# Kernel optimization log

Hardware: AMD Instinct MI355X
Metric: run time of the kernel (lower is better)

Reference implementation:

```python
import jax, jax.numpy as jnp
import numpy as np

E, H, I, T, K = 8, 2048, 1024, 4096, 2
GROUP = 32


def dequant_int4(packed, scale, group):
    """packed: [E, R, C//2] ints in [0,256) holding two 4-bit values per byte.
    scale: [E, R, C//group]. Returns fp32 [E, R, C] with w = (nibble - 8) * scale."""
    lo = (packed & 0xF) - 8          # even columns
    hi = ((packed >> 4) & 0xF) - 8   # odd columns
    e, r, ch = packed.shape
    w = jnp.stack([lo, hi], axis=-1).reshape(e, r, 2 * ch).astype(jnp.float32)
    w = w.reshape(e, r, -1, group) * scale[..., None]
    return w.reshape(e, r, 2 * ch)


def setup_inputs() -> dict:
    key = jax.random.key(0)
    ks = jax.random.split(key, 6)
    x = jax.random.normal(ks[0], (T, H), dtype=jnp.float32)
    w1 = jax.random.randint(ks[1], (E, 2 * I, H // 2), 0, 256, dtype=jnp.int32)
    w1_scale = jax.random.uniform(ks[2], (E, 2 * I, H // GROUP), dtype=jnp.float32) * 0.02
    w2 = jax.random.randint(ks[3], (E, H, I // 2), 0, 256, dtype=jnp.int32)
    w2_scale = jax.random.uniform(ks[4], (E, H, I // GROUP), dtype=jnp.float32) * 0.02
    logits = jax.random.normal(ks[5], (T, E), dtype=jnp.float32)
    top_vals, top_idx = jax.lax.top_k(logits, K)
    expert_weights = jax.nn.softmax(top_vals, axis=-1)   # [T, K]
    expert_indices = top_idx.astype(jnp.int32)           # [T, K]
    return {"x": x, "w1": w1, "w1_scale": w1_scale, "w2": w2,
            "w2_scale": w2_scale, "expert_weights": expert_weights,
            "expert_indices": expert_indices, "top_k": K}


def reference(x, w1, w1_scale, w2, w2_scale, expert_weights, expert_indices, top_k):
    inter = w2.shape[2] * 2
    W1 = dequant_int4(w1, w1_scale, GROUP)   # [E, 2I, H]
    W2 = dequant_int4(w2, w2_scale, GROUP)   # [E, H, I]
    y13 = jnp.einsum('th,erh->etr', x, W1)   # [E, T, 2I]
    gate, up = y13[..., :inter], y13[..., inter:]
    h = jax.nn.silu(gate) * up               # [E, T, I] SwiGLU
    y = jnp.einsum('eti,ehi->eth', h, W2)    # [E, T, H]
    t_ids = jnp.arange(x.shape[0])[:, None]  # [T, 1]
    sel = y[expert_indices, t_ids, :]        # [T, K, H]
    return jnp.einsum('tkh,tk->th', sel, expert_weights)
```

## Files before the change

kernel.cpp:

```cpp
#include <hip/hip_runtime.h>
#include <cstdint>
#include <cstddef>

typedef unsigned int u32;
typedef unsigned short u16;
typedef __bf16 bf16x8 __attribute__((ext_vector_type(8)));
typedef float f32x4 __attribute__((ext_vector_type(4)));
typedef u16 u16x8 __attribute__((ext_vector_type(8)));

static constexpr int T_TOK = 4096;
static constexpr int HID   = 2048;
static constexpr int INTER = 1024;
static constexpr int NEXP  = 8;
static constexpr int TOPK  = 2;
static constexpr int SLOT_CAP = 10240;
static constexpr int NT_M = 40;

static constexpr int M_TOT  = 16;
static constexpr int M_CUR  = 17;
static constexpr int M_DONE = 40;
static constexpr int M_TOK  = 96;

__device__ __forceinline__ u16 f2bf(float f) {
  u32 u = __builtin_bit_cast(u32, f);
  u32 r = (u + 0x7fffu + ((u >> 16) & 1u)) >> 16;
  return (u16)r;
}
__device__ __forceinline__ float bf2f(u16 h) {
  return __builtin_bit_cast(float, (u32)h << 16);
}

__device__ __forceinline__ void spin_ge(int* p, int target) {
  while (__hip_atomic_load(p, __ATOMIC_RELAXED, __HIP_MEMORY_SCOPE_AGENT) < target)
    __builtin_amdgcn_s_sleep(8);
  __builtin_amdgcn_fence(__ATOMIC_ACQUIRE, "agent");
}
__device__ __forceinline__ void bump(int* p, int tid) {
  __syncthreads();
  if (tid == 0)
    __hip_atomic_fetch_add(p, 1, __ATOMIC_RELEASE, __HIP_MEMORY_SCOPE_AGENT);
}

__global__ void router_count(const int* __restrict__ eidx, int* __restrict__ meta) {
  __shared__ int cnt[NEXP];
  const int tid = threadIdx.x;
  if (tid < NEXP) cnt[tid] = 0;
  __syncthreads();
  for (int i = tid; i < T_TOK * TOPK; i += 256) atomicAdd(&cnt[eidx[i]], 1);
  __syncthreads();
  if (tid == 0) {
    int off = 0;
    for (int e = 0; e < NEXP; ++e) {
      int c = cnt[e];
      meta[e] = c;
      meta[8 + e] = off;
      meta[M_CUR + e] = off;
      off += (c + 255) & ~255;
    }
    meta[M_TOT] = off;
  }
}

__global__ void init_k(int* __restrict__ meta) {
  const int i = blockIdx.x * 256 + threadIdx.x;
  if (i < SLOT_CAP) meta[M_TOK + i] = 0;
  if (i >= 25 && i < 80) meta[i] = 0;
}

__global__ void router_assign(const int* __restrict__ eidx, int* __restrict__ meta) {
  const int t = blockIdx.x * 256 + threadIdx.x;
  if (t >= T_TOK) return;
  int* cursors = meta + M_CUR;
  int* toklist = meta + M_TOK;
  for (int k = 0; k < TOPK; ++k) {
    const int e = eidx[t * TOPK + k];
    const int pos = atomicAdd(&cursors[e], 1);
    toklist[pos] = t * 2 + k;
  }
}

template <int CPR>
__device__ __forceinline__ void deq1(const int* __restrict__ p, const float* __restrict__ s,
                                     u16* __restrict__ w, int gid) {
  const int row = gid / CPR;
  const int cid = gid % CPR;
  const int4 pk = *(const int4*)(p + (size_t)gid * 4);
  const float sc = s[(size_t)row * (CPR / 4) + (cid >> 2)];
  int v[4] = {pk.x, pk.y, pk.z, pk.w};
  u16x8 o;
#pragma unroll
  for (int b = 0; b < 4; ++b) {
    o[2 * b]     = f2bf((float)((v[b] & 15) - 8) * sc);
    o[2 * b + 1] = f2bf((float)(((v[b] >> 4) & 15) - 8) * sc);
  }
  *(u16x8*)(w + (size_t)gid * 8) = o;
}

__global__ void prep_k(const int* __restrict__ w1, const float* __restrict__ w1s,
                       const int* __restrict__ w2, const float* __restrict__ w2s,
                       const float* __restrict__ x, u16* __restrict__ W1b,
                       u16* __restrict__ W2b, u16* __restrict__ xb) {
  const int blk = blockIdx.x;
  if (blk < 16384) {
    deq1<256>(w1, w1s, W1b, blk * 256 + threadIdx.x);
  } else if (blk < 24576) {
    deq1<128>(w2, w2s, W2b, (blk - 16384) * 256 + threadIdx.x);
  } else {
    const int i = ((blk - 24576) * 256 + threadIdx.x) * 8;
    const float4 a = *(const float4*)(x + i);
    const float4 b = *(const float4*)(x + i + 4);
    u16x8 o;
    o[0] = f2bf(a.x); o[1] = f2bf(a.y); o[2] = f2bf(a.z); o[3] = f2bf(a.w);
    o[4] = f2bf(b.x); o[5] = f2bf(b.y); o[6] = f2bf(b.z); o[7] = f2bf(b.w);
    *(u16x8*)(xb + i) = o;
  }
}

template <int KT, bool G1M>
__device__ void gemm_body(const u16* __restrict__ A, const u16* __restrict__ Be,
                          u16* __restrict__ Cout, const int* __restrict__ toklist,
                          int vend, u16* lds, int slot0, int nt, int tid) {
  static constexpr int NT = KT / 64;
  char* ldsB = (char*)lds;

  const u16* asrc[4];
  const u16* bsrc[4];
#pragma unroll
  for (int j = 0; j < 4; ++j) {
    const int L = j * 8192 + tid * 16;
    const int S = L >> 10;
    int o = L & 1023;
    o ^= ((o >> 7) & 3) << 4;
    const int r = (S >> 1) * 16 + (o >> 6);
    const int cb = (S & 1) * 64 + (o & 63);
    const int arow = G1M ? (toklist[slot0 + r] >> 1) : (slot0 + r);
    asrc[j] = A + (size_t)arow * KT + (cb >> 1);
    int brow;
    if (G1M) {
      const int g = r >> 6, j6 = r & 63;
      brow = nt * 128 + g * 32 + (j6 & 31) + ((j6 >> 5) << 10);
    } else {
      brow = nt * 256 + r;
    }
    bsrc[j] = Be + (size_t)brow * KT + (cb >> 1);
  }

#define STAGE(kt_, c_)                                                                \
  do {                                                                                \
    char* dA_ = ldsB + (c_) * 65536;                                                  \
    char* dB_ = dA_ + 32768;                                                          \
    _Pragma("unroll") for (int j = 0; j < 4; ++j)                                     \
        __builtin_amdgcn_global_load_lds(                                             \
            (const __attribute__((address_space(1))) void*)(asrc[j] + (kt_) * 64),    \
            (__attribute__((address_space(3))) void*)(dA_ + j * 8192 + tid * 16),     \
            16, 0, 0);                                                                \
    _Pragma("unroll") for (int j = 0; j < 4; ++j)                                     \
        __builtin_amdgcn_global_load_lds(                                             \
            (const __attribute__((address_space(1))) void*)(bsrc[j] + (kt_) * 64),    \
            (__attribute__((address_space(3))) void*)(dB_ + j * 8192 + tid * 16),     \
            16, 0, 0);                                                                \
  } while (0)

  const int lane = tid & 63;
  const int wid = tid >> 6;
  const int wm = (wid >> 2) * 128;
  const int wn = (wid & 3) * 64;
  const int fr = lane & 15;
  const int qq = lane >> 4;
  const int swz = (qq * 16) ^ (((fr >> 1) & 3) << 4);

  const int abase = (wm >> 4) * 2048 + fr * 64 + swz;
  const int bbase = 32768 + (wn >> 4) * 2048 + fr * 64 + swz;

  f32x4 acc[8][4];
#pragma unroll
  for (int m = 0; m < 8; ++m)
#pragma unroll
    for (int n = 0; n < 4; ++n) acc[m][n] = (f32x4)0.0f;

#define COMPUTE(c_)                                                                   \
  do {                                                                                \
    const char* bb_ = ldsB + (c_) * 65536;                                            \
    bf16x8 bfr_[4][2];                                                                \
    _Pragma("unroll") for (int nf = 0; nf < 4; ++nf)                                  \
        _Pragma("unroll") for (int ks = 0; ks < 2; ++ks)                              \
            bfr_[nf][ks] = *(const bf16x8*)(bb_ + bbase + nf * 2048 + ks * 1024);     \
    _Pragma("unroll") for (int mh = 0; mh < 2; ++mh) {                                \
      bf16x8 af_[4][2];                                                               \
      _Pragma("unroll") for (int mf = 0; mf < 4; ++mf)                                \
          _Pragma("unroll") for (int ks = 0; ks < 2; ++ks)                            \
              af_[mf][ks] = *(const bf16x8*)(bb_ + abase + mh * 8192 + mf * 2048 +    \
                                             ks * 1024);                              \
      __builtin_amdgcn_s_setprio(1);                                                  \
      _Pragma("unroll") for (int mf = 0; mf < 4; ++mf)                                \
          _Pragma("unroll") for (int nf = 0; nf < 4; ++nf)                            \
              _Pragma("unroll") for (int ks = 0; ks < 2; ++ks)                        \
                  acc[mh * 4 + mf][nf] = __builtin_amdgcn_mfma_f32_16x16x32_bf16(     \
                      af_[mf][ks], bfr_[nf][ks], acc[mh * 4 + mf][nf], 0, 0, 0);      \
      __builtin_amdgcn_s_setprio(0);                                                  \
    }                                                                                 \
  } while (0)

  STAGE(0, 0);
#pragma unroll 1
  for (int kt = 0; kt < NT; kt += 2) {
    asm volatile("s_waitcnt vmcnt(0)" ::: "memory");
    __builtin_amdgcn_s_barrier();
    __builtin_amdgcn_sched_barrier(0);
    if (kt + 1 < NT) STAGE(kt + 1, 1);
    COMPUTE(0);
    asm volatile("s_waitcnt vmcnt(0)" ::: "memory");
    __builtin_amdgcn_s_barrier();
    __builtin_amdgcn_sched_barrier(0);
    if (kt + 2 < NT) STAGE(kt + 2, 0);
    COMPUTE(1);
  }
#undef STAGE
#undef COMPUTE

  if (G1M) {
    const int g = wid & 3;
#pragma unroll
    for (int mi = 0; mi < 8; ++mi)
#pragma unroll
      for (int n = 0; n < 2; ++n)
#pragma unroll
        for (int jj = 0; jj < 4; ++jj) {
          const float gv = acc[mi][n][jj];
          const float uv = acc[mi][n + 2][jj];
          const float hv = gv / (1.0f + __expf(-gv)) * uv;
          const int row = slot0 + wm + mi * 16 + qq * 4 + jj;
          Cout[(size_t)row * INTER + nt * 128 + g * 32 + n * 16 + fr] = f2bf(hv);
        }
  } else {
#pragma unroll
    for (int mi = 0; mi < 8; ++mi)
#pragma unroll
      for (int jj = 0; jj < 4; ++jj) {
        const int slot = slot0 + wm + mi * 16 + qq * 4 + jj;
        if (slot < vend) {
          const int tk = toklist[slot];
          const int col = nt * 256 + wn + fr;
#pragma unroll
          for (int n = 0; n < 4; ++n)
            Cout[(size_t)tk * HID + col + n * 16] = f2bf(acc[mi][n][jj]);
        }
      }
  }
}

__device__ __forceinline__ void run_g1(const u16* xb, const u16* W1b, u16* hbuf,
                                       int* meta, const int* toklist, u16* lds,
                                       int mt, int nt, int tid) {
  const int slot0 = mt * 256;
  if (slot0 < meta[M_TOT]) {
    int e = 0;
#pragma unroll
    for (int i = 1; i < NEXP; ++i) e += (slot0 >= meta[8 + i]);
    gemm_body<2048, true>(xb, W1b + (size_t)e * 2048 * 2048, hbuf, toklist, 0,
                          lds, slot0, nt, tid);
  }
  bump(&meta[M_DONE + mt], tid);
}

__device__ __forceinline__ void run_g2(const u16* hbuf, const u16* W2b, u16* yt,
                                       int* meta, const int* toklist, u16* lds,
                                       int mt, int nt, int tid) {
  const int slot0 = mt * 256;
  if (slot0 >= meta[M_TOT]) return;
  int e = 0;
#pragma unroll
  for (int i = 1; i < NEXP; ++i) e += (slot0 >= meta[8 + i]);
  if (tid == 0) spin_ge(&meta[M_DONE + mt], 8);
  __syncthreads();
  const int vend = meta[8 + e] + meta[e];
  gemm_body<1024, false>(hbuf, W2b + (size_t)e * 2048 * 1024, yt, toklist, vend,
                         lds, slot0, nt, tid);
}

__global__ __launch_bounds__(512, 2) void gemm_static(
    const u16* __restrict__ xb, const u16* __restrict__ W1b,
    const u16* __restrict__ W2b, u16* __restrict__ hbuf, u16* __restrict__ yt,
    int* __restrict__ meta) {
  __shared__ u16 lds[2 * 32768];
  const int tid = threadIdx.x;
  const int b = blockIdx.x;
  const int* toklist = meta + M_TOK;

  run_g1(xb, W1b, hbuf, meta, toklist, lds, b & 31, b >> 5, tid);
  if (b < 64) {
    run_g1(xb, W1b, hbuf, meta, toklist, lds, 32 + (b & 7), b >> 3, tid);
    run_g2(hbuf, W2b, yt, meta, toklist, lds, 32 + (b & 7), b >> 3, tid);
  } else {
    const int x = b & 7, q = (b - 64) >> 3;
    {
      const int k = q;
      run_g2(hbuf, W2b, yt, meta, toklist, lds, x + 8 * (k & 3), k >> 2, tid);
    }
    if (q < 8) {
      const int k = q + 24;
      run_g2(hbuf, W2b, yt, meta, toklist, lds, x + 8 * (k & 3), k >> 2, tid);
    }
  }
}

__global__ void combine_k(const u16* __restrict__ yt, const float* __restrict__ ew,
                          float* __restrict__ out) {
  const int idx = blockIdx.x * 256 + threadIdx.x;
  const int t = idx >> 8;
  const int pos = (idx & 255) * 8;
  const float w0 = ew[t * 2];
  const float w1 = ew[t * 2 + 1];
  const u16x8 v0 = *(const u16x8*)(yt + (size_t)(t * 2) * HID + pos);
  const u16x8 v1 = *(const u16x8*)(yt + (size_t)(t * 2 + 1) * HID + pos);
  float* dst = out + (size_t)t * HID + pos;
  float4 o0, o1;
  o0.x = w0 * bf2f(v0[0]) + w1 * bf2f(v1[0]);
  o0.y = w0 * bf2f(v0[1]) + w1 * bf2f(v1[1]);
  o0.z = w0 * bf2f(v0[2]) + w1 * bf2f(v1[2]);
  o0.w = w0 * bf2f(v0[3]) + w1 * bf2f(v1[3]);
  o1.x = w0 * bf2f(v0[4]) + w1 * bf2f(v1[4]);
  o1.y = w0 * bf2f(v0[5]) + w1 * bf2f(v1[5]);
  o1.z = w0 * bf2f(v0[6]) + w1 * bf2f(v1[6]);
  o1.w = w0 * bf2f(v0[7]) + w1 * bf2f(v1[7]);
  *(float4*)dst = o0;
  *(float4*)(dst + 4) = o1;
}

extern "C" void kernel_launch(void* const* d_in, const int* in_sizes, int n_in,
                              void* d_out, int out_size, void* d_ws, size_t ws_size,
                              hipStream_t stream) {
  const float* x    = (const float*)d_in[0];
  const int*   w1   = (const int*)d_in[1];
  const float* w1s  = (const float*)d_in[2];
  const int*   w2   = (const int*)d_in[3];
  const float* w2s  = (const float*)d_in[4];
  const float* ew   = (const float*)d_in[5];
  const int*   eidx = (const int*)d_in[6];
  float* out = (float*)d_out;

  char* ws = (char*)d_ws;
  const size_t OFF_W1B  = 0;
  const size_t OFF_W2B  = 67108864;
  const size_t OFF_XB   = 100663296;
  const size_t OFF_H    = 117440512;
  const size_t OFF_YT   = 138412032;
  const size_t OFF_META = 171966464;
  const size_t NEED     = 172043264;
  if (ws_size < NEED) return;

  u16* W1b  = (u16*)(ws + OFF_W1B);
  u16* W2b  = (u16*)(ws + OFF_W2B);
  u16* xb   = (u16*)(ws + OFF_XB);
  u16* hbuf = (u16*)(ws + OFF_H);
  u16* yt   = (u16*)(ws + OFF_YT);
  int* meta = (int*)(ws + OFF_META);

  router_count<<<1, 256, 0, stream>>>(eidx, meta);
  init_k<<<SLOT_CAP / 256, 256, 0, stream>>>(meta);
  router_assign<<<T_TOK / 256, 256, 0, stream>>>(eidx, meta);

  prep_k<<<28672, 256, 0, stream>>>(w1, w1s, w2, w2s, x, W1b, W2b, xb);

  gemm_static<<<256, 512, 0, stream>>>(xb, W1b, W2b, hbuf, yt, meta);

  combine_k<<<(T_TOK * HID) / (256 * 8), 256, 0, stream>>>(yt, ew, out);
}
```

Baseline: 251.8 us.

## Interleave global-to-LDS staging with MFMA sub-blocks in ping-pong schedule

Replaces the two-stage loop (stage next tile, then compute the whole tile) with a finer schedule. Each k-tile's compute is split into four MFMA quarter blocks, with barriers between them, and the global_load_lds issues for the next tiles are spread across those quarters. Two tiles are prefetched up front and partial vmcnt waits are used, so memory traffic overlaps more evenly with matrix work. The loop now always issues loads with wrapped indices (masked by NT-1), which assumes NT is a power of two and adds redundant trailing loads. It also adds many more barriers.

```diff
diff --git a/kernel.cpp b/kernel.cpp
--- a/kernel.cpp
+++ b/kernel.cpp
@@ -145,21 +145,18 @@
     bsrc[j] = Be + (size_t)brow * KT + (cb >> 1);
   }
 
-#define STAGE(kt_, c_)                                                                \
-  do {                                                                                \
-    char* dA_ = ldsB + (c_) * 65536;                                                  \
-    char* dB_ = dA_ + 32768;                                                          \
-    _Pragma("unroll") for (int j = 0; j < 4; ++j)                                     \
-        __builtin_amdgcn_global_load_lds(                                             \
-            (const __attribute__((address_space(1))) void*)(asrc[j] + (kt_) * 64),    \
-            (__attribute__((address_space(3))) void*)(dA_ + j * 8192 + tid * 16),     \
-            16, 0, 0);                                                                \
-    _Pragma("unroll") for (int j = 0; j < 4; ++j)                                     \
-        __builtin_amdgcn_global_load_lds(                                             \
-            (const __attribute__((address_space(1))) void*)(bsrc[j] + (kt_) * 64),    \
-            (__attribute__((address_space(3))) void*)(dB_ + j * 8192 + tid * 16),     \
-            16, 0, 0);                                                                \
-  } while (0)
+#define STG_A(kt_, c_, j_)                                                          \
+  __builtin_amdgcn_global_load_lds(                                                 \
+      (const __attribute__((address_space(1))) void*)(asrc[j_] + (kt_) * 64),       \
+      (__attribute__((address_space(3))) void*)(ldsB + (c_) * 65536 + (j_) * 8192 + \
+                                                tid * 16),                           \
+      16, 0, 0)
+#define STG_B(kt_, c_, j_)                                                          \
+  __builtin_amdgcn_global_load_lds(                                                 \
+      (const __attribute__((address_space(1))) void*)(bsrc[j_] + (kt_) * 64),       \
+      (__attribute__((address_space(3))) void*)(ldsB + (c_) * 65536 + 32768 +       \
+                                                (j_) * 8192 + tid * 16),             \
+      16, 0, 0)
 
   const int lane = tid & 63;
   const int wid = tid >> 6;
@@ -178,45 +175,76 @@
 #pragma unroll
     for (int n = 0; n < 4; ++n) acc[m][n] = (f32x4)0.0f;
 
-#define COMPUTE(c_)                                                                   \
-  do {                                                                                \
-    const char* bb_ = ldsB + (c_) * 65536;                                            \
-    bf16x8 bfr_[4][2];                                                                \
-    _Pragma("unroll") for (int nf = 0; nf < 4; ++nf)                                  \
-        _Pragma("unroll") for (int ks = 0; ks < 2; ++ks)                              \
-            bfr_[nf][ks] = *(const bf16x8*)(bb_ + bbase + nf * 2048 + ks * 1024);     \
-    _Pragma("unroll") for (int mh = 0; mh < 2; ++mh) {                                \
-      bf16x8 af_[4][2];                                                               \
-      _Pragma("unroll") for (int mf = 0; mf < 4; ++mf)                                \
-          _Pragma("unroll") for (int ks = 0; ks < 2; ++ks)                            \
-              af_[mf][ks] = *(const bf16x8*)(bb_ + abase + mh * 8192 + mf * 2048 +    \
-                                             ks * 1024);                              \
-      __builtin_amdgcn_s_setprio(1);                                                  \
-      _Pragma("unroll") for (int mf = 0; mf < 4; ++mf)                                \
-          _Pragma("unroll") for (int nf = 0; nf < 4; ++nf)                            \
-              _Pragma("unroll") for (int ks = 0; ks < 2; ++ks)                        \
-                  acc[mh * 4 + mf][nf] = __builtin_amdgcn_mfma_f32_16x16x32_bf16(     \
-                      af_[mf][ks], bfr_[nf][ks], acc[mh * 4 + mf][nf], 0, 0, 0);      \
-      __builtin_amdgcn_s_setprio(0);                                                  \
-    }                                                                                 \
+  bf16x8 af[4][2], b01[2][2], b23[2][2];
+
+#define BARRIER asm volatile("s_barrier" ::: "memory")
+#define LGKM0                                              \
+  do {                                                     \
+    asm volatile("s_waitcnt lgkmcnt(0)" ::: "memory");     \
+    __builtin_amdgcn_sched_barrier(0);                     \
   } while (0)
-
-  STAGE(0, 0);
+#define DS_AF(c_, mh_)                                                              \
+  _Pragma("unroll") for (int mf = 0; mf < 4; ++mf)                                  \
+  _Pragma("unroll") for (int ks = 0; ks < 2; ++ks)                                  \
+      af[mf][ks] = *(const bf16x8*)(ldsB + (c_) * 65536 + abase + (mh_) * 8192 +    \
+                                    mf * 2048 + ks * 1024);
+#define DS_B(c_, bh_, BV_)                                                          \
+  _Pragma("unroll") for (int nf = 0; nf < 2; ++nf)                                  \
+  _Pragma("unroll") for (int ks = 0; ks < 2; ++ks)                                  \
+      BV_[nf][ks] = *(const bf16x8*)(ldsB + (c_) * 65536 + bbase +                  \
+                                     ((bh_) * 2 + nf) * 2048 + ks * 1024);
+#define MFMA16(mh_, bh_, BV_)                                                       \
+  do {                                                                              \
+    __builtin_amdgcn_s_setprio(1);                                                  \
+    _Pragma("unroll") for (int mf = 0; mf < 4; ++mf)                                \
+    _Pragma("unroll") for (int nf = 0; nf < 2; ++nf)                                \
+    _Pragma("unroll") for (int ks = 0; ks < 2; ++ks)                                \
+        acc[(mh_) * 4 + mf][(bh_) * 2 + nf] =                                       \
+            __builtin_amdgcn_mfma_f32_16x16x32_bf16(                                \
+                af[mf][ks], BV_[nf][ks], acc[(mh_) * 4 + mf][(bh_) * 2 + nf],       \
+                0, 0, 0);                                                           \
+    __builtin_amdgcn_s_setprio(0);                                                  \
+  } while (0)
+
+  STG_A(0, 0, 0); STG_A(0, 0, 2); STG_B(0, 0, 0); STG_B(0, 0, 1);
+  STG_B(0, 0, 2); STG_B(0, 0, 3); STG_A(0, 0, 1); STG_A(0, 0, 3);
+  STG_A(1, 1, 0); STG_A(1, 1, 2); STG_B(1, 1, 0); STG_B(1, 1, 1);
+  STG_B(1, 1, 2); STG_B(1, 1, 3); STG_A(1, 1, 1); STG_A(1, 1, 3);
+  asm volatile("s_waitcnt vmcnt(8)" ::: "memory");
+  BARRIER;
+
 #pragma unroll 1
-  for (int kt = 0; kt < NT; kt += 2) {
-    asm volatile("s_waitcnt vmcnt(0)" ::: "memory");
-    __builtin_amdgcn_s_barrier();
-    __builtin_amdgcn_sched_barrier(0);
-    if (kt + 1 < NT) STAGE(kt + 1, 1);
-    COMPUTE(0);
-    asm volatile("s_waitcnt vmcnt(0)" ::: "memory");
-    __builtin_amdgcn_s_barrier();
-    __builtin_amdgcn_sched_barrier(0);
-    if (kt + 2 < NT) STAGE(kt + 2, 0);
-    COMPUTE(1);
-  }
-#undef STAGE
-#undef COMPUTE
+  for (int it = 0; it < NT / 2; ++it) {
+    const int s0 = (2 * it + 2) & (NT - 1);
+    const int s1 = (2 * it + 3) & (NT - 1);
+    DS_AF(0, 0); DS_B(0, 0, b01);
+    BARRIER; LGKM0; MFMA16(0, 0, b01); BARRIER;
+    DS_B(0, 1, b23); STG_A(s0, 0, 0); STG_A(s0, 0, 2);
+    BARRIER; LGKM0; MFMA16(0, 1, b23); BARRIER;
+    DS_AF(0, 1); STG_B(s0, 0, 0); STG_B(s0, 0, 1);
+    BARRIER; LGKM0; MFMA16(1, 0, b01); BARRIER;
+    STG_B(s0, 0, 2); STG_B(s0, 0, 3);
+    BARRIER; MFMA16(1, 1, b23);
+    asm volatile("s_waitcnt vmcnt(6)" ::: "memory");
+    BARRIER;
+    DS_AF(1, 0); DS_B(1, 0, b01); STG_A(s0, 0, 1); STG_A(s0, 0, 3);
+    BARRIER; LGKM0; MFMA16(0, 0, b01); BARRIER;
+    DS_B(1, 1, b23); STG_A(s1, 1, 0); STG_A(s1, 1, 2);
+    BARRIER; LGKM0; MFMA16(0, 1, b23); BARRIER;
+    DS_AF(1, 1); STG_B(s1, 1, 0); STG_B(s1, 1, 1); STG_B(s1, 1, 2); STG_B(s1, 1, 3);
+    BARRIER; LGKM0; MFMA16(1, 0, b01); BARRIER;
+    STG_A(s1, 1, 1); STG_A(s1, 1, 3);
+    BARRIER; MFMA16(1, 1, b23);
+    asm volatile("s_waitcnt vmcnt(8)" ::: "memory");
+    BARRIER;
+  }
+#undef STG_A
+#undef STG_B
+#undef BARRIER
+#undef LGKM0
+#undef DS_AF
+#undef DS_B
+#undef MFMA16
 
   if (G1M) {
     const int g = wid & 3;
```

Result: no change. 256.1 us (+1.7%).

## Shrink fused MoE GEMM tiles to 128x128 with one-shot grid and per-tile sync

Applied to the files above, without the earlier changes.

Replaces the persistent 256-block, 256x256-tile schedule with a one-shot grid of 128x128 tiles on 256-thread blocks. Each block runs its gate/up GEMM tile, then waits on a per-row-tile counter before its down-projection tile. Expert slot padding drops from 256 to 128, which cuts wasted rows and exposes more parallel blocks. In exchange, the double-buffered LDS pipeline and MFMA priority hints are removed in favour of a single buffer with two barriers per k-step, so load latency is no longer hidden. Smaller tiles also give less operand reuse, and spinning blocks hold CU slots while they wait.

```diff
diff --git a/kernel.cpp b/kernel.cpp
--- a/kernel.cpp
+++ b/kernel.cpp
@@ -13,13 +13,14 @@
 static constexpr int INTER = 1024;
 static constexpr int NEXP  = 8;
 static constexpr int TOPK  = 2;
-static constexpr int SLOT_CAP = 10240;
-static constexpr int NT_M = 40;
+static constexpr int SLOT_CAP = 9216;
+static constexpr int NT_M = 72;
+static constexpr int NT_N = 16;
 
 static constexpr int M_TOT  = 16;
 static constexpr int M_CUR  = 17;
-static constexpr int M_DONE = 40;
-static constexpr int M_TOK  = 96;
+static constexpr int M_DONE = 128;
+static constexpr int M_TOK  = 256;
 
 __device__ __forceinline__ u16 f2bf(float f) {
   u32 u = __builtin_bit_cast(u32, f);
@@ -55,7 +56,7 @@
       meta[e] = c;
       meta[8 + e] = off;
       meta[M_CUR + e] = off;
-      off += (c + 255) & ~255;
+      off += (c + 127) & ~127;
     }
     meta[M_TOT] = off;
   }
@@ -64,7 +65,7 @@
 __global__ void init_k(int* __restrict__ meta) {
   const int i = blockIdx.x * 256 + threadIdx.x;
   if (i < SLOT_CAP) meta[M_TOK + i] = 0;
-  if (i >= 25 && i < 80) meta[i] = 0;
+  if (i >= M_DONE && i < M_DONE + NT_M) meta[i] = 0;
 }
 
 __global__ void router_assign(const int* __restrict__ eidx, int* __restrict__ meta) {
@@ -117,9 +118,9 @@
 }
 
 template <int KT, bool G1M>
-__device__ void gemm_body(const u16* __restrict__ A, const u16* __restrict__ Be,
-                          u16* __restrict__ Cout, const int* __restrict__ toklist,
-                          int vend, u16* lds, int slot0, int nt, int tid) {
+__device__ void tile128(const u16* __restrict__ A, const u16* __restrict__ Be,
+                        u16* __restrict__ Cout, const int* __restrict__ toklist,
+                        int vend, u16* lds, int slot0, int nt, int tid) {
   static constexpr int NT = KT / 64;
   char* ldsB = (char*)lds;
 
@@ -127,7 +128,7 @@
   const u16* bsrc[4];
 #pragma unroll
   for (int j = 0; j < 4; ++j) {
-    const int L = j * 8192 + tid * 16;
+    const int L = j * 4096 + tid * 16;
     const int S = L >> 10;
     int o = L & 1023;
     o ^= ((o >> 7) & 3) << 4;
@@ -137,171 +138,126 @@
     asrc[j] = A + (size_t)arow * KT + (cb >> 1);
     int brow;
     if (G1M) {
-      const int g = r >> 6, j6 = r & 63;
-      brow = nt * 128 + g * 32 + (j6 & 31) + ((j6 >> 5) << 10);
+      const int w = r >> 6, j6 = r & 63;
+      brow = (j6 < 32) ? (nt * 64 + w * 32 + j6)
+                       : (1024 + nt * 64 + w * 32 + (j6 & 31));
     } else {
-      brow = nt * 256 + r;
+      brow = nt * 128 + r;
     }
     bsrc[j] = Be + (size_t)brow * KT + (cb >> 1);
   }
 
-#define STAGE(kt_, c_)                                                                \
-  do {                                                                                \
-    char* dA_ = ldsB + (c_) * 65536;                                                  \
-    char* dB_ = dA_ + 32768;                                                          \
-    _Pragma("unroll") for (int j = 0; j < 4; ++j)                                     \
-        __builtin_amdgcn_global_load_lds(                                             \
-            (const __attribute__((address_space(1))) void*)(asrc[j] + (kt_) * 64),    \
-            (__attribute__((address_space(3))) void*)(dA_ + j * 8192 + tid * 16),     \
-            16, 0, 0);                                                                \
-    _Pragma("unroll") for (int j = 0; j < 4; ++j)                                     \
-        __builtin_amdgcn_global_load_lds(                                             \
-            (const __attribute__((address_space(1))) void*)(bsrc[j] + (kt_) * 64),    \
-            (__attribute__((address_space(3))) void*)(dB_ + j * 8192 + tid * 16),     \
-            16, 0, 0);                                                                \
-  } while (0)
-
   const int lane = tid & 63;
   const int wid = tid >> 6;
-  const int wm = (wid >> 2) * 128;
-  const int wn = (wid & 3) * 64;
+  const int wm = (wid >> 1) * 64;
+  const int wn = (wid & 1) * 64;
   const int fr = lane & 15;
   const int qq = lane >> 4;
   const int swz = (qq * 16) ^ (((fr >> 1) & 3) << 4);
 
   const int abase = (wm >> 4) * 2048 + fr * 64 + swz;
-  const int bbase = 32768 + (wn >> 4) * 2048 + fr * 64 + swz;
-
-  f32x4 acc[8][4];
-#pragma unroll
-  for (int m = 0; m < 8; ++m)
+  const int bbase = 16384 + (wn >> 4) * 2048 + fr * 64 + swz;
+
+  f32x4 acc[4][4];
+#pragma unroll
+  for (int m = 0; m < 4; ++m)
 #pragma unroll
     for (int n = 0; n < 4; ++n) acc[m][n] = (f32x4)0.0f;
 
-#define COMPUTE(c_)                                                                   \
-  do {                                                                                \
-    const char* bb_ = ldsB + (c_) * 65536;                                            \
-    bf16x8 bfr_[4][2];                                                                \
-    _Pragma("unroll") for (int nf = 0; nf < 4; ++nf)                                  \
-        _Pragma("unroll") for (int ks = 0; ks < 2; ++ks)                              \
-            bfr_[nf][ks] = *(const bf16x8*)(bb_ + bbase + nf * 2048 + ks * 1024);     \
-    _Pragma("unroll") for (int mh = 0; mh < 2; ++mh) {                                \
-      bf16x8 af_[4][2];                                                               \
-      _Pragma("unroll") for (int mf = 0; mf < 4; ++mf)                                \
-          _Pragma("unroll") for (int ks = 0; ks < 2; ++ks)                            \
-              af_[mf][ks] = *(const bf16x8*)(bb_ + abase + mh * 8192 + mf * 2048 +    \
-                                             ks * 1024);                              \
-      __builtin_amdgcn_s_setprio(1);                                                  \
-      _Pragma("unroll") for (int mf = 0; mf < 4; ++mf)                                \
-          _Pragma("unroll") for (int nf = 0; nf < 4; ++nf)                            \
-              _Pragma("unroll") for (int ks = 0; ks < 2; ++ks)                        \
-                  acc[mh * 4 + mf][nf] = __builtin_amdgcn_mfma_f32_16x16x32_bf16(     \
-                      af_[mf][ks], bfr_[nf][ks], acc[mh * 4 + mf][nf], 0, 0, 0);      \
-      __builtin_amdgcn_s_setprio(0);                                                  \
-    }                                                                                 \
-  } while (0)
-
-  STAGE(0, 0);
 #pragma unroll 1
-  for (int kt = 0; kt < NT; kt += 2) {
-    asm volatile("s_waitcnt vmcnt(0)" ::: "memory");
-    __builtin_amdgcn_s_barrier();
-    __builtin_amdgcn_sched_barrier(0);
-    if (kt + 1 < NT) STAGE(kt + 1, 1);
-    COMPUTE(0);
-    asm volatile("s_waitcnt vmcnt(0)" ::: "memory");
-    __builtin_amdgcn_s_barrier();
-    __builtin_amdgcn_sched_barrier(0);
-    if (kt + 2 < NT) STAGE(kt + 2, 0);
-    COMPUTE(1);
-  }
-#undef STAGE
-#undef COMPUTE
+  for (int kt = 0; kt < NT; ++kt) {
+    __syncthreads();
+#pragma unroll
+    for (int j = 0; j < 4; ++j) {
+      __builtin_amdgcn_global_load_lds(
+          (const __attribute__((address_space(1))) void*)(asrc[j] + kt * 64),
+          (__attribute__((address_space(3))) void*)(ldsB + j * 4096 + tid * 16),
+          16, 0, 0);
+      __builtin_amdgcn_global_load_lds(
+          (const __attribute__((address_space(1))) void*)(bsrc[j] + kt * 64),
+          (__attribute__((address_space(3))) void*)(ldsB + 16384 + j * 4096 + tid * 16),
+          16, 0, 0);
+    }
+    __syncthreads();
+#pragma unroll
+    for (int ks = 0; ks < 2; ++ks) {
+      bf16x8 a[4], b[4];
+#pragma unroll
+      for (int m = 0; m < 4; ++m)
+        a[m] = *(const bf16x8*)(ldsB + abase + m * 2048 + ks * 1024);
+#pragma unroll
+      for (int n = 0; n < 4; ++n)
+        b[n] = *(const bf16x8*)(ldsB + bbase + n * 2048 + ks * 1024);
+#pragma unroll
+      for (int m = 0; m < 4; ++m)
+#pragma unroll
+        for (int n = 0; n < 4; ++n)
+          acc[m][n] = __builtin_amdgcn_mfma_f32_16x16x32_bf16(a[m], b[n], acc[m][n], 0, 0, 0);
+    }
+  }
 
   if (G1M) {
-    const int g = wid & 3;
-#pragma unroll
-    for (int mi = 0; mi < 8; ++mi)
+    const int g = wid & 1;
+#pragma unroll
+    for (int m = 0; m < 4; ++m)
 #pragma unroll
       for (int n = 0; n < 2; ++n)
 #pragma unroll
         for (int jj = 0; jj < 4; ++jj) {
-          const float gv = acc[mi][n][jj];
-          const float uv = acc[mi][n + 2][jj];
+          const float gv = acc[m][n][jj];
+          const float uv = acc[m][n + 2][jj];
           const float hv = gv / (1.0f + __expf(-gv)) * uv;
-          const int row = slot0 + wm + mi * 16 + qq * 4 + jj;
-          Cout[(size_t)row * INTER + nt * 128 + g * 32 + n * 16 + fr] = f2bf(hv);
+          const int row = slot0 + wm + m * 16 + qq * 4 + jj;
+          Cout[(size_t)row * INTER + nt * 64 + g * 32 + n * 16 + fr] = f2bf(hv);
         }
   } else {
 #pragma unroll
-    for (int mi = 0; mi < 8; ++mi)
+    for (int m = 0; m < 4; ++m)
 #pragma unroll
       for (int jj = 0; jj < 4; ++jj) {
-        const int slot = slot0 + wm + mi * 16 + qq * 4 + jj;
+        const int slot = slot0 + wm + m * 16 + qq * 4 + jj;
         if (slot < vend) {
           const int tk = toklist[slot];
-          const int col = nt * 256 + wn + fr;
+          const int col = nt * 128 + wn + fr;
 #pragma unroll
           for (int n = 0; n < 4; ++n)
-            Cout[(size_t)tk * HID + col + n * 16] = f2bf(acc[mi][n][jj]);
+            Cout[(size_t)tk * HID + col + n * 16] = f2bf(acc[m][n][jj]);
         }
       }
   }
 }
 
-__device__ __forceinline__ void run_g1(const u16* xb, const u16* W1b, u16* hbuf,
-                                       int* meta, const int* toklist, u16* lds,
-                                       int mt, int nt, int tid) {
-  const int slot0 = mt * 256;
-  if (slot0 < meta[M_TOT]) {
-    int e = 0;
-#pragma unroll
-    for (int i = 1; i < NEXP; ++i) e += (slot0 >= meta[8 + i]);
-    gemm_body<2048, true>(xb, W1b + (size_t)e * 2048 * 2048, hbuf, toklist, 0,
-                          lds, slot0, nt, tid);
-  }
-  bump(&meta[M_DONE + mt], tid);
-}
-
-__device__ __forceinline__ void run_g2(const u16* hbuf, const u16* W2b, u16* yt,
-                                       int* meta, const int* toklist, u16* lds,
-                                       int mt, int nt, int tid) {
-  const int slot0 = mt * 256;
-  if (slot0 >= meta[M_TOT]) return;
-  int e = 0;
-#pragma unroll
-  for (int i = 1; i < NEXP; ++i) e += (slot0 >= meta[8 + i]);
-  if (tid == 0) spin_ge(&meta[M_DONE + mt], 8);
-  __syncthreads();
-  const int vend = meta[8 + e] + meta[e];
-  gemm_body<1024, false>(hbuf, W2b + (size_t)e * 2048 * 1024, yt, toklist, vend,
-                         lds, slot0, nt, tid);
-}
-
-__global__ __launch_bounds__(512, 2) void gemm_static(
+__global__ __launch_bounds__(256, 2) void gemm_fused(
     const u16* __restrict__ xb, const u16* __restrict__ W1b,
     const u16* __restrict__ W2b, u16* __restrict__ hbuf, u16* __restrict__ yt,
     int* __restrict__ meta) {
-  __shared__ u16 lds[2 * 32768];
+  __shared__ u16 lds[16384];
   const int tid = threadIdx.x;
-  const int b = blockIdx.x;
+  const int j = blockIdx.x;
+  const int mt = j >> 4, nt = j & 15;
+  const int slot0 = mt * 128;
   const int* toklist = meta + M_TOK;
-
-  run_g1(xb, W1b, hbuf, meta, toklist, lds, b & 31, b >> 5, tid);
-  if (b < 64) {
-    run_g1(xb, W1b, hbuf, meta, toklist, lds, 32 + (b & 7), b >> 3, tid);
-    run_g2(hbuf, W2b, yt, meta, toklist, lds, 32 + (b & 7), b >> 3, tid);
-  } else {
-    const int x = b & 7, q = (b - 64) >> 3;
-    {
-      const int k = q;
-      run_g2(hbuf, W2b, yt, meta, toklist, lds, x + 8 * (k & 3), k >> 2, tid);
-    }
-    if (q < 8) {
-      const int k = q + 24;
-      run_g2(hbuf, W2b, yt, meta, toklist, lds, x + 8 * (k & 3), k >> 2, tid);
-    }
-  }
+  const int tot = meta[M_TOT];
+
+  if (slot0 < tot) {
+    int e = 0;
+#pragma unroll
+    for (int i = 1; i < NEXP; ++i) e += (slot0 >= meta[8 + i]);
+    tile128<2048, true>(xb, W1b + (size_t)e * 2048 * 2048, hbuf, toklist, 0,
+                        lds, slot0, nt, tid);
+  }
+  bump(&meta[M_DONE + mt], tid);
+  if (slot0 >= tot) return;
+
+  if (tid == 0) spin_ge(&meta[M_DONE + mt], 16);
+  __syncthreads();
+
+  int e = 0;
+#pragma unroll
+  for (int i = 1; i < NEXP; ++i) e += (slot0 >= meta[8 + i]);
+  const int vend = meta[8 + e] + meta[e];
+  tile128<1024, false>(hbuf, W2b + (size_t)e * 2048 * 1024, yt, toklist, vend,
+                       lds, slot0, nt, tid);
 }
 
 __global__ void combine_k(const u16* __restrict__ yt, const float* __restrict__ ew,
@@ -362,7 +318,7 @@
 
   prep_k<<<28672, 256, 0, stream>>>(w1, w1s, w2, w2s, x, W1b, W2b, xb);
 
-  gemm_static<<<256, 512, 0, stream>>>(xb, W1b, W2b, hbuf, yt, meta);
+  gemm_fused<<<NT_M * NT_N, 256, 0, stream>>>(xb, W1b, W2b, hbuf, yt, meta);
 
   combine_k<<<(T_TOK * HID) / (256 * 8), 256, 0, stream>>>(yt, ew, out);
 }
```

Result: slower. 324.9 us (+29.0%).

## Gather activations into slot order during prep and keep expert outputs slot-ordered

Applied to the files above, without the earlier changes.

The prep kernel now converts x to bf16 already permuted into expert-slot order, so GEMM1 reads contiguous rows with no toklist lookup. GEMM2 writes its outputs straight to slot-ordered rows, and combine finds each token's rows through a new slot-of map built by the router. The output buffer reuses the gathered-x buffer. That is safe only because GEMM2 on a row tile waits until every GEMM1 tile reading those rows has finished. The cost is converting and writing padded slots (about 2.5x the rows of x) in prep, in exchange for plain addressing inside both GEMMs.

```diff
diff --git a/kernel.cpp b/kernel.cpp
--- a/kernel.cpp
+++ b/kernel.cpp
@@ -16,10 +16,11 @@
 static constexpr int SLOT_CAP = 10240;
 static constexpr int NT_M = 40;
 
-static constexpr int M_TOT  = 16;
-static constexpr int M_CUR  = 17;
-static constexpr int M_DONE = 40;
-static constexpr int M_TOK  = 96;
+static constexpr int M_TOT    = 16;
+static constexpr int M_CUR    = 17;
+static constexpr int M_DONE   = 40;
+static constexpr int M_TOK    = 96;
+static constexpr int M_SLOTOF = 96 + SLOT_CAP;
 
 __device__ __forceinline__ u16 f2bf(float f) {
   u32 u = __builtin_bit_cast(u32, f);
@@ -72,10 +73,12 @@
   if (t >= T_TOK) return;
   int* cursors = meta + M_CUR;
   int* toklist = meta + M_TOK;
+  int* slotof  = meta + M_SLOTOF;
   for (int k = 0; k < TOPK; ++k) {
     const int e = eidx[t * TOPK + k];
     const int pos = atomicAdd(&cursors[e], 1);
     toklist[pos] = t * 2 + k;
+    slotof[t * 2 + k] = pos;
   }
 }
 
@@ -99,27 +102,29 @@
 __global__ void prep_k(const int* __restrict__ w1, const float* __restrict__ w1s,
                        const int* __restrict__ w2, const float* __restrict__ w2s,
                        const float* __restrict__ x, u16* __restrict__ W1b,
-                       u16* __restrict__ W2b, u16* __restrict__ xb) {
+                       u16* __restrict__ W2b, u16* __restrict__ xs,
+                       const int* __restrict__ meta) {
   const int blk = blockIdx.x;
   if (blk < 16384) {
     deq1<256>(w1, w1s, W1b, blk * 256 + threadIdx.x);
   } else if (blk < 24576) {
     deq1<128>(w2, w2s, W2b, (blk - 16384) * 256 + threadIdx.x);
   } else {
-    const int i = ((blk - 24576) * 256 + threadIdx.x) * 8;
-    const float4 a = *(const float4*)(x + i);
-    const float4 b = *(const float4*)(x + i + 4);
+    const int slot = blk - 24576;
+    const int tok = meta[M_TOK + slot] >> 1;
+    const float* src = x + (size_t)tok * HID + threadIdx.x * 8;
+    const float4 a = *(const float4*)src;
+    const float4 b = *(const float4*)(src + 4);
     u16x8 o;
     o[0] = f2bf(a.x); o[1] = f2bf(a.y); o[2] = f2bf(a.z); o[3] = f2bf(a.w);
     o[4] = f2bf(b.x); o[5] = f2bf(b.y); o[6] = f2bf(b.z); o[7] = f2bf(b.w);
-    *(u16x8*)(xb + i) = o;
+    *(u16x8*)(xs + (size_t)slot * HID + threadIdx.x * 8) = o;
   }
 }
 
 template <int KT, bool G1M>
 __device__ void gemm_body(const u16* __restrict__ A, const u16* __restrict__ Be,
-                          u16* __restrict__ Cout, const int* __restrict__ toklist,
-                          int vend, u16* lds, int slot0, int nt, int tid) {
+                          u16* __restrict__ Cout, u16* lds, int slot0, int nt, int tid) {
   static constexpr int NT = KT / 64;
   char* ldsB = (char*)lds;
 
@@ -133,8 +138,7 @@
     o ^= ((o >> 7) & 3) << 4;
     const int r = (S >> 1) * 16 + (o >> 6);
     const int cb = (S & 1) * 64 + (o & 63);
-    const int arow = G1M ? (toklist[slot0 + r] >> 1) : (slot0 + r);
-    asrc[j] = A + (size_t)arow * KT + (cb >> 1);
+    asrc[j] = A + (size_t)(slot0 + r) * KT + (cb >> 1);
     int brow;
     if (G1M) {
       const int g = r >> 6, j6 = r & 63;
@@ -237,35 +241,29 @@
     for (int mi = 0; mi < 8; ++mi)
 #pragma unroll
       for (int jj = 0; jj < 4; ++jj) {
-        const int slot = slot0 + wm + mi * 16 + qq * 4 + jj;
-        if (slot < vend) {
-          const int tk = toklist[slot];
-          const int col = nt * 256 + wn + fr;
-#pragma unroll
-          for (int n = 0; n < 4; ++n)
-            Cout[(size_t)tk * HID + col + n * 16] = f2bf(acc[mi][n][jj]);
-        }
+        const int row = slot0 + wm + mi * 16 + qq * 4 + jj;
+        const int col = nt * 256 + wn + fr;
+#pragma unroll
+        for (int n = 0; n < 4; ++n)
+          Cout[(size_t)row * HID + col + n * 16] = f2bf(acc[mi][n][jj]);
       }
   }
 }
 
-__device__ __forceinline__ void run_g1(const u16* xb, const u16* W1b, u16* hbuf,
-                                       int* meta, const int* toklist, u16* lds,
-                                       int mt, int nt, int tid) {
+__device__ __forceinline__ void run_g1(const u16* xs, const u16* W1b, u16* hbuf,
+                                       int* meta, u16* lds, int mt, int nt, int tid) {
   const int slot0 = mt * 256;
   if (slot0 < meta[M_TOT]) {
     int e = 0;
 #pragma unroll
     for (int i = 1; i < NEXP; ++i) e += (slot0 >= meta[8 + i]);
-    gemm_body<2048, true>(xb, W1b + (size_t)e * 2048 * 2048, hbuf, toklist, 0,
-                          lds, slot0, nt, tid);
+    gemm_body<2048, true>(xs, W1b + (size_t)e * 2048 * 2048, hbuf, lds, slot0, nt, tid);
   }
   bump(&meta[M_DONE + mt], tid);
 }
 
-__device__ __forceinline__ void run_g2(const u16* hbuf, const u16* W2b, u16* yt,
-                                       int* meta, const int* toklist, u16* lds,
-                                       int mt, int nt, int tid) {
+__device__ __forceinline__ void run_g2(const u16* hbuf, const u16* W2b, u16* ys,
+                                       int* meta, u16* lds, int mt, int nt, int tid) {
   const int slot0 = mt * 256;
   if (slot0 >= meta[M_TOT]) return;
   int e = 0;
@@ -273,46 +271,46 @@
   for (int i = 1; i < NEXP; ++i) e += (slot0 >= meta[8 + i]);
   if (tid == 0) spin_ge(&meta[M_DONE + mt], 8);
   __syncthreads();
-  const int vend = meta[8 + e] + meta[e];
-  gemm_body<1024, false>(hbuf, W2b + (size_t)e * 2048 * 1024, yt, toklist, vend,
-                         lds, slot0, nt, tid);
+  gemm_body<1024, false>(hbuf, W2b + (size_t)e * 2048 * 1024, ys, lds, slot0, nt, tid);
 }
 
 __global__ __launch_bounds__(512, 2) void gemm_static(
-    const u16* __restrict__ xb, const u16* __restrict__ W1b,
-    const u16* __restrict__ W2b, u16* __restrict__ hbuf, u16* __restrict__ yt,
+    const u16* __restrict__ xs, const u16* __restrict__ W1b,
+    const u16* __restrict__ W2b, u16* __restrict__ hbuf, u16* __restrict__ ys,
     int* __restrict__ meta) {
   __shared__ u16 lds[2 * 32768];
   const int tid = threadIdx.x;
   const int b = blockIdx.x;
-  const int* toklist = meta + M_TOK;
-
-  run_g1(xb, W1b, hbuf, meta, toklist, lds, b & 31, b >> 5, tid);
+
+  run_g1(xs, W1b, hbuf, meta, lds, b & 31, b >> 5, tid);
   if (b < 64) {
-    run_g1(xb, W1b, hbuf, meta, toklist, lds, 32 + (b & 7), b >> 3, tid);
-    run_g2(hbuf, W2b, yt, meta, toklist, lds, 32 + (b & 7), b >> 3, tid);
+    run_g1(xs, W1b, hbuf, meta, lds, 32 + (b & 7), b >> 3, tid);
+    run_g2(hbuf, W2b, ys, meta, lds, 32 + (b & 7), b >> 3, tid);
   } else {
     const int x = b & 7, q = (b - 64) >> 3;
     {
       const int k = q;
-      run_g2(hbuf, W2b, yt, meta, toklist, lds, x + 8 * (k & 3), k >> 2, tid);
+      run_g2(hbuf, W2b, ys, meta, lds, x + 8 * (k & 3), k >> 2, tid);
     }
     if (q < 8) {
       const int k = q + 24;
-      run_g2(hbuf, W2b, yt, meta, toklist, lds, x + 8 * (k & 3), k >> 2, tid);
+      run_g2(hbuf, W2b, ys, meta, lds, x + 8 * (k & 3), k >> 2, tid);
     }
   }
 }
 
-__global__ void combine_k(const u16* __restrict__ yt, const float* __restrict__ ew,
-                          float* __restrict__ out) {
+__global__ void combine_k(const u16* __restrict__ ys, const float* __restrict__ ew,
+                          const int* __restrict__ meta, float* __restrict__ out) {
   const int idx = blockIdx.x * 256 + threadIdx.x;
   const int t = idx >> 8;
   const int pos = (idx & 255) * 8;
+  const int* slotof = meta + M_SLOTOF;
+  const int s0 = slotof[t * 2];
+  const int s1 = slotof[t * 2 + 1];
   const float w0 = ew[t * 2];
   const float w1 = ew[t * 2 + 1];
-  const u16x8 v0 = *(const u16x8*)(yt + (size_t)(t * 2) * HID + pos);
-  const u16x8 v1 = *(const u16x8*)(yt + (size_t)(t * 2 + 1) * HID + pos);
+  const u16x8 v0 = *(const u16x8*)(ys + (size_t)s0 * HID + pos);
+  const u16x8 v1 = *(const u16x8*)(ys + (size_t)s1 * HID + pos);
   float* dst = out + (size_t)t * HID + pos;
   float4 o0, o1;
   o0.x = w0 * bf2f(v0[0]) + w1 * bf2f(v1[0]);
@@ -342,27 +340,25 @@
   char* ws = (char*)d_ws;
   const size_t OFF_W1B  = 0;
   const size_t OFF_W2B  = 67108864;
-  const size_t OFF_XB   = 100663296;
-  const size_t OFF_H    = 117440512;
-  const size_t OFF_YT   = 138412032;
-  const size_t OFF_META = 171966464;
-  const size_t NEED     = 172043264;
+  const size_t OFF_XS   = 100663296;
+  const size_t OFF_H    = 142606336;
+  const size_t OFF_META = 163577856;
+  const size_t NEED     = 163708928;
   if (ws_size < NEED) return;
 
   u16* W1b  = (u16*)(ws + OFF_W1B);
   u16* W2b  = (u16*)(ws + OFF_W2B);
-  u16* xb   = (u16*)(ws + OFF_XB);
+  u16* xs   = (u16*)(ws + OFF_XS);
   u16* hbuf = (u16*)(ws + OFF_H);
-  u16* yt   = (u16*)(ws + OFF_YT);
   int* meta = (int*)(ws + OFF_META);
 
   router_count<<<1, 256, 0, stream>>>(eidx, meta);
   init_k<<<SLOT_CAP / 256, 256, 0, stream>>>(meta);
   router_assign<<<T_TOK / 256, 256, 0, stream>>>(eidx, meta);
 
-  prep_k<<<28672, 256, 0, stream>>>(w1, w1s, w2, w2s, x, W1b, W2b, xb);
-
-  gemm_static<<<256, 512, 0, stream>>>(xb, W1b, W2b, hbuf, yt, meta);
-
-  combine_k<<<(T_TOK * HID) / (256 * 8), 256, 0, stream>>>(yt, ew, out);
-}
+  prep_k<<<34816, 256, 0, stream>>>(w1, w1s, w2, w2s, x, W1b, W2b, xs, meta);
+
+  gemm_static<<<256, 512, 0, stream>>>(xs, W1b, W2b, hbuf, xs, meta);
+
+  combine_k<<<(T_TOK * HID) / (256 * 8), 256, 0, stream>>>(xs, ew, meta, out);
+}
```

Measured after the change: 254.3 us. Within noise of the previous version (+1.0%).
